# Optimization experiments

Hardware: AMD Instinct MI355X
Metric: run time of the kernel (lower is better)

The kernel has to match this reference:

```python
import jax, jax.numpy as jnp
import numpy as np

B = 131072
SD, AD, HID = 24, 8, 32
NH = SD + AD            # n_heads = 32
UNITS = HID * NH        # 1024


def _xavier(k, shape):
    fan_in, fan_out = shape[-2], shape[-1]
    lim = float(np.sqrt(6.0 / (fan_in + fan_out)))
    return jax.random.uniform(k, shape, jnp.float32, -lim, lim)


def setup_inputs() -> dict:
    key = jax.random.key(0)
    ks = jax.random.split(key, 8)
    return dict(
        state=jax.random.normal(ks[0], (B, SD), jnp.float32),
        action=jax.random.normal(ks[1], (B, AD), jnp.float32),
        # ripple layer 1: per-head Linear(NH -> HID), gate logits init 0 (init_prob=0.5)
        W1=_xavier(ks[2], (NH, NH, HID)), b1=jnp.zeros((NH, HID), jnp.float32), g1=jnp.zeros((NH,), jnp.float32),
        # ripple layer 2: per-head Linear(UNITS -> HID)
        W2=_xavier(ks[3], (NH, UNITS, HID)), b2=jnp.zeros((NH, HID), jnp.float32), g2=jnp.zeros((NH,), jnp.float32),
        # q_network
        Wq1=_xavier(ks[4], (UNITS, 256)), bq1=jnp.zeros((256,), jnp.float32),
        ln1_g=jnp.ones((256,), jnp.float32), ln1_b=jnp.zeros((256,), jnp.float32),
        Wq2=_xavier(ks[5], (256, 128)), bq2=jnp.zeros((128,), jnp.float32),
        ln2_g=jnp.ones((128,), jnp.float32), ln2_b=jnp.zeros((128,), jnp.float32),
        Wq3=_xavier(ks[6], (128, 1)), bq3=jnp.zeros((1,), jnp.float32),
    )


def _ripple(x, W, b, g):
    # x: [B, D]; W: [H, D, K]; per-head linear + tanh, scaled by per-head sigmoid gate
    h = jnp.tanh(jnp.einsum('bd,hdk->bhk', x, W) + b[None])  # [B, H, K]
    h = h * jax.nn.sigmoid(g)[None, :, None]
    return h.reshape(x.shape[0], -1)  # [B, H*K]


def _ln(x, g, b, eps=1e-5):
    mu = jnp.mean(x, -1, keepdims=True)
    var = jnp.mean((x - mu) ** 2, -1, keepdims=True)
    return (x - mu) * jax.lax.rsqrt(var + eps) * g + b


def reference(state, action, W1, b1, g1, W2, b2, g2,
              Wq1, bq1, ln1_g, ln1_b, Wq2, bq2, ln2_g, ln2_b, Wq3, bq3):
    sa = jnp.concatenate([state, action], axis=1)          # [B, SD+AD]
    x = _ripple(sa, W1, b1, g1)                            # [B, UNITS]
    x = _ripple(x, W2, b2, g2)                             # [B, UNITS]
    h = jax.nn.relu(_ln(x @ Wq1 + bq1, ln1_g, ln1_b))      # [B, 256] (dropout = eval identity)
    h = jax.nn.relu(_ln(h @ Wq2 + bq2, ln2_g, ln2_b))      # [B, 128]
    return h @ Wq3 + bq3                                   # [B, 1]
```

## Files before the change

### kernel.cpp

```cpp
#include <hip/hip_runtime.h>
#include <hip/hip_bf16.h>

typedef _Float16 f16x8 __attribute__((ext_vector_type(8)));
typedef float f32x4 __attribute__((ext_vector_type(4)));

__device__ __forceinline__ void async16(const _Float16* g, _Float16* l) {
  __builtin_amdgcn_global_load_lds(
      (const __attribute__((address_space(1))) unsigned int*)g,
      (__attribute__((address_space(3))) unsigned int*)l, 16, 0, 0);
}

__device__ __forceinline__ float tanh_fast(float x) {
  float e = __expf(2.0f * x);
  return 1.0f - 2.0f * __builtin_amdgcn_rcpf(e + 1.0f);
}
__device__ __forceinline__ float sigmoid_fast(float x) {
  return __builtin_amdgcn_rcpf(1.0f + __expf(-x));
}

__global__ __launch_bounds__(256) void transpose_cvt(const float* __restrict__ in,
                                                     _Float16* __restrict__ out,
                                                     int R, int C) {
  __shared__ float tile[32][33];
  int z = blockIdx.z;
  in  += (size_t)z * R * C;
  out += (size_t)z * R * C;
  int r0 = blockIdx.x * 32, c0 = blockIdx.y * 32;
  int t = threadIdx.x;
  int cc = t & 31, rr8 = t >> 5;
#pragma unroll
  for (int p = 0; p < 4; ++p) {
    int r = rr8 + p * 8;
    tile[cc][r] = in[(size_t)(r0 + r) * C + c0 + cc];
  }
  __syncthreads();
  int rr = t & 31, cc8 = t >> 5;
#pragma unroll
  for (int p = 0; p < 4; ++p) {
    int c = cc8 + p * 8;
    out[(size_t)(c0 + c) * R + r0 + rr] = (_Float16)tile[c][rr];
  }
}

__global__ __launch_bounds__(256) void k1_ripple1(
    const float* __restrict__ state, const float* __restrict__ action,
    const _Float16* __restrict__ v1t, const float* __restrict__ b1,
    const float* __restrict__ g1, _Float16* __restrict__ x1, int gro) {
  __shared__ __align__(16) _Float16 As[128 * 40];
  int bn = blockIdx.x, bm = blockIdx.y;
  int t = threadIdx.x, w = t >> 6, l = t & 63, q = l >> 4, l15 = l & 15;
  int n0 = bn * 128, m0 = bm * 128;

  {
    int r = t >> 1, half = t & 1;
    size_t grow = (size_t)(gro + m0 + r);
    float v[16];
    if (half == 0) {
      const float4* sp = (const float4*)(state + grow * 24);
      ((float4*)v)[0] = sp[0]; ((float4*)v)[1] = sp[1];
      ((float4*)v)[2] = sp[2]; ((float4*)v)[3] = sp[3];
    } else {
      const float4* sp = (const float4*)(state + grow * 24 + 16);
      ((float4*)v)[0] = sp[0]; ((float4*)v)[1] = sp[1];
      const float4* ap = (const float4*)(action + grow * 8);
      ((float4*)v)[2] = ap[0]; ((float4*)v)[3] = ap[1];
    }
    f16x8 h0, h1;
#pragma unroll
    for (int j = 0; j < 8; ++j) { h0[j] = (_Float16)v[j]; h1[j] = (_Float16)v[8 + j]; }
    *(f16x8*)&As[r * 40 + half * 16] = h0;
    *(f16x8*)&As[r * 40 + half * 16 + 8] = h1;
  }
  __syncthreads();

  int wr = w >> 1, wc = w & 1;
  f16x8 af[4], bf[4];
#pragma unroll
  for (int mi = 0; mi < 4; ++mi)
    af[mi] = *(const f16x8*)&As[(wr * 64 + mi * 16 + l15) * 40 + q * 8];
#pragma unroll
  for (int ni = 0; ni < 4; ++ni)
    bf[ni] = *(const f16x8*)(v1t + (size_t)(n0 + wc * 64 + ni * 16 + l15) * 32 + q * 8);

  f32x4 acc[4][4] = {};
#pragma unroll
  for (int mi = 0; mi < 4; ++mi)
#pragma unroll
    for (int ni = 0; ni < 4; ++ni)
      acc[mi][ni] = __builtin_amdgcn_mfma_f32_16x16x32_f16(af[mi], bf[ni], acc[mi][ni], 0, 0, 0);

#pragma unroll
  for (int ni = 0; ni < 4; ++ni) {
    int col = n0 + wc * 64 + ni * 16 + l15;
    float sg = sigmoid_fast(g1[col >> 5]);
    float bias = b1[col];
#pragma unroll
    for (int mi = 0; mi < 4; ++mi)
#pragma unroll
      for (int r = 0; r < 4; ++r) {
        int row = m0 + wr * 64 + mi * 16 + q * 4 + r;
        x1[(size_t)row * 1024 + col] = (_Float16)(tanh_fast(acc[mi][ni][r] + bias) * sg);
      }
  }
}

__global__ __launch_bounds__(256, 2) void k2_ripple2(
    const _Float16* __restrict__ x1, const _Float16* __restrict__ v2t,
    const float* __restrict__ b2, const float* __restrict__ g2,
    _Float16* __restrict__ x2, int nbm) {
  __shared__ __align__(16) _Float16 As[128 * 32];
  __shared__ __align__(16) _Float16 Bs[256 * 32];
  int g = blockIdx.x;
  int bn, bm;
  if ((nbm & 7) == 0) {
    int x = g & 7, j = g >> 3;
    bn = j & 3; bm = x + 8 * (j >> 2);
  } else { bn = g & 3; bm = g >> 2; }
  int t = threadIdx.x, w = t >> 6, l = t & 63, q = l >> 4, l15 = l & 15;
  int n0 = bn * 256, m0 = bm * 128;
  int wr = w >> 1, wc = w & 1;
  f32x4 acc[4][8] = {};

  int cA0 = t, cA1 = t + 256;
  const _Float16* aS0 = x1 + (size_t)(m0 + (cA0 >> 2)) * 1024 + ((cA0 & 3) ^ ((cA0 >> 3) & 3)) * 8;
  const _Float16* aS1 = x1 + (size_t)(m0 + (cA1 >> 2)) * 1024 + ((cA1 & 3) ^ ((cA1 >> 3) & 3)) * 8;
  _Float16* aD0 = As + cA0 * 8;
  _Float16* aD1 = As + cA1 * 8;
  const _Float16* bS[4]; _Float16* bD[4];
#pragma unroll
  for (int i = 0; i < 4; ++i) {
    int c = t + i * 256;
    bS[i] = v2t + (size_t)(n0 + (c >> 2)) * 1024 + ((c & 3) ^ ((c >> 3) & 3)) * 8;
    bD[i] = Bs + c * 8;
  }
  int qs = q ^ ((l15 >> 1) & 3);

  for (int kt = 0; kt < 32; ++kt) {
    __syncthreads();
    int ko = kt * 32;
    async16(aS0 + ko, aD0);
    async16(aS1 + ko, aD1);
#pragma unroll
    for (int i = 0; i < 4; ++i) async16(bS[i] + ko, bD[i]);
    __builtin_amdgcn_s_waitcnt(0);
    __syncthreads();
    f16x8 af[4], bf[8];
#pragma unroll
    for (int mi = 0; mi < 4; ++mi)
      af[mi] = *(const f16x8*)&As[(wr * 64 + mi * 16 + l15) * 32 + qs * 8];
#pragma unroll
    for (int ni = 0; ni < 8; ++ni)
      bf[ni] = *(const f16x8*)&Bs[(wc * 128 + ni * 16 + l15) * 32 + qs * 8];
#pragma unroll
    for (int mi = 0; mi < 4; ++mi)
#pragma unroll
      for (int ni = 0; ni < 8; ++ni)
        acc[mi][ni] = __builtin_amdgcn_mfma_f32_16x16x32_f16(af[mi], bf[ni], acc[mi][ni], 0, 0, 0);
  }

#pragma unroll
  for (int ni = 0; ni < 8; ++ni) {
    int col = n0 + wc * 128 + ni * 16 + l15;
    float sg = sigmoid_fast(g2[col >> 5]);
    float bias = b2[col];
#pragma unroll
    for (int mi = 0; mi < 4; ++mi)
#pragma unroll
      for (int r = 0; r < 4; ++r) {
        int row = m0 + wr * 64 + mi * 16 + q * 4 + r;
        x2[(size_t)row * 1024 + col] = (_Float16)(tanh_fast(acc[mi][ni][r] + bias) * sg);
      }
  }
}

__global__ __launch_bounds__(256) void k3_head(
    const _Float16* __restrict__ x2, const _Float16* __restrict__ t1t,
    const _Float16* __restrict__ t2t,
    const float* __restrict__ bq1, const float* __restrict__ ln1g, const float* __restrict__ ln1b,
    const float* __restrict__ bq2, const float* __restrict__ ln2g, const float* __restrict__ ln2b,
    const float* __restrict__ wq3, const float* __restrict__ bq3,
    float* __restrict__ out) {
  __shared__ __align__(16) _Float16 Ast[64 * 32];
  __shared__ __align__(16) _Float16 Bst[256 * 32];
  __shared__ __align__(16) _Float16 y1h[64 * 264];
  __shared__ float redA[64 * 4], redB[64 * 4];
  __shared__ float meanv[64], rstdv[64];
  int bm = blockIdx.x;
  int t = threadIdx.x, w = t >> 6, l = t & 63, q = l >> 4, l15 = l & 15;
  int m0 = bm * 64;
  int qs = q ^ ((l15 >> 1) & 3);

  f32x4 acc[4][4] = {};
  int cA = t;
  const _Float16* aS = x2 + (size_t)(m0 + (cA >> 2)) * 1024 + ((cA & 3) ^ ((cA >> 3) & 3)) * 8;
  _Float16* aD = Ast + cA * 8;
  const _Float16* bS[4]; _Float16* bD[4];
#pragma unroll
  for (int i = 0; i < 4; ++i) {
    int c = t + i * 256;
    bS[i] = t1t + (size_t)(c >> 2) * 1024 + ((c & 3) ^ ((c >> 3) & 3)) * 8;
    bD[i] = Bst + c * 8;
  }

  for (int kt = 0; kt < 32; ++kt) {
    __syncthreads();
    int ko = kt * 32;
    async16(aS + ko, aD);
#pragma unroll
    for (int i = 0; i < 4; ++i) async16(bS[i] + ko, bD[i]);
    __builtin_amdgcn_s_waitcnt(0);
    __syncthreads();
    f16x8 af[4], bf[4];
#pragma unroll
    for (int mi = 0; mi < 4; ++mi)
      af[mi] = *(const f16x8*)&Ast[(mi * 16 + l15) * 32 + qs * 8];
#pragma unroll
    for (int ni = 0; ni < 4; ++ni)
      bf[ni] = *(const f16x8*)&Bst[(w * 64 + ni * 16 + l15) * 32 + qs * 8];
#pragma unroll
    for (int mi = 0; mi < 4; ++mi)
#pragma unroll
      for (int ni = 0; ni < 4; ++ni)
        acc[mi][ni] = __builtin_amdgcn_mfma_f32_16x16x32_f16(af[mi], bf[ni], acc[mi][ni], 0, 0, 0);
  }

#pragma unroll
  for (int ni = 0; ni < 4; ++ni) {
    int col = w * 64 + ni * 16 + l15;
    float b = bq1[col];
#pragma unroll
    for (int mi = 0; mi < 4; ++mi)
#pragma unroll
      for (int r = 0; r < 4; ++r) acc[mi][ni][r] += b;
  }
#pragma unroll
  for (int mi = 0; mi < 4; ++mi)
#pragma unroll
    for (int r = 0; r < 4; ++r) {
      int row = mi * 16 + q * 4 + r;
      float s = 0.f, sq = 0.f;
#pragma unroll
      for (int ni = 0; ni < 4; ++ni) { float v = acc[mi][ni][r]; s += v; sq += v * v; }
#pragma unroll
      for (int off = 1; off < 16; off <<= 1) { s += __shfl_xor(s, off); sq += __shfl_xor(sq, off); }
      if (l15 == 0) { redA[row * 4 + w] = s; redB[row * 4 + w] = sq; }
    }
  __syncthreads();
  if (t < 64) {
    float s  = redA[t * 4] + redA[t * 4 + 1] + redA[t * 4 + 2] + redA[t * 4 + 3];
    float sq = redB[t * 4] + redB[t * 4 + 1] + redB[t * 4 + 2] + redB[t * 4 + 3];
    float mean = s * (1.0f / 256.0f);
    float var = sq * (1.0f / 256.0f) - mean * mean;
    meanv[t] = mean; rstdv[t] = rsqrtf(var + 1e-5f);
  }
  __syncthreads();
#pragma unroll
  for (int mi = 0; mi < 4; ++mi)
#pragma unroll
    for (int ni = 0; ni < 4; ++ni)
#pragma unroll
      for (int r = 0; r < 4; ++r) {
        int row = mi * 16 + q * 4 + r;
        int col = w * 64 + ni * 16 + l15;
        float y = (acc[mi][ni][r] - meanv[row]) * rstdv[row] * ln1g[col] + ln1b[col];
        y = fmaxf(y, 0.f);
        y1h[row * 264 + col] = (_Float16)y;
      }
  __syncthreads();

  int wr = w >> 1, wc = w & 1;
  f32x4 a2[2][4] = {};
  for (int kt = 0; kt < 8; ++kt) {
    f16x8 af2[2];
#pragma unroll
    for (int mi = 0; mi < 2; ++mi)
      af2[mi] = *(const f16x8*)&y1h[(wr * 32 + mi * 16 + l15) * 264 + kt * 32 + q * 8];
#pragma unroll
    for (int ni = 0; ni < 4; ++ni) {
      f16x8 bf = *(const f16x8*)(t2t + (size_t)(wc * 64 + ni * 16 + l15) * 256 + kt * 32 + q * 8);
#pragma unroll
      for (int mi = 0; mi < 2; ++mi)
        a2[mi][ni] = __builtin_amdgcn_mfma_f32_16x16x32_f16(af2[mi], bf, a2[mi][ni], 0, 0, 0);
    }
  }
#pragma unroll
  for (int ni = 0; ni < 4; ++ni) {
    int col = wc * 64 + ni * 16 + l15;
    float b = bq2[col];
#pragma unroll
    for (int mi = 0; mi < 2; ++mi)
#pragma unroll
      for (int r = 0; r < 4; ++r) a2[mi][ni][r] += b;
  }
  __syncthreads();
#pragma unroll
  for (int mi = 0; mi < 2; ++mi)
#pragma unroll
    for (int r = 0; r < 4; ++r) {
      int row = wr * 32 + mi * 16 + q * 4 + r;
      float s = 0.f, sq = 0.f;
#pragma unroll
      for (int ni = 0; ni < 4; ++ni) { float v = a2[mi][ni][r]; s += v; sq += v * v; }
#pragma unroll
      for (int off = 1; off < 16; off <<= 1) { s += __shfl_xor(s, off); sq += __shfl_xor(sq, off); }
      if (l15 == 0) { redA[row * 2 + wc] = s; redB[row * 2 + wc] = sq; }
    }
  __syncthreads();
  if (t < 64) {
    float s = redA[t * 2] + redA[t * 2 + 1];
    float sq = redB[t * 2] + redB[t * 2 + 1];
    float mean = s * (1.0f / 128.0f);
    float var = sq * (1.0f / 128.0f) - mean * mean;
    meanv[t] = mean; rstdv[t] = rsqrtf(var + 1e-5f);
  }
  __syncthreads();
#pragma unroll
  for (int mi = 0; mi < 2; ++mi)
#pragma unroll
    for (int r = 0; r < 4; ++r) {
      int row = wr * 32 + mi * 16 + q * 4 + r;
      float pr = 0.f;
#pragma unroll
      for (int ni = 0; ni < 4; ++ni) {
        int col = wc * 64 + ni * 16 + l15;
        float y = (a2[mi][ni][r] - meanv[row]) * rstdv[row] * ln2g[col] + ln2b[col];
        y = fmaxf(y, 0.f);
        pr += y * wq3[col];
      }
#pragma unroll
      for (int off = 1; off < 16; off <<= 1) pr += __shfl_xor(pr, off);
      if (l15 == 0) redA[row * 2 + wc] = pr;
    }
  __syncthreads();
  if (t < 64) out[m0 + t] = redA[t * 2] + redA[t * 2 + 1] + bq3[0];
}

extern "C" void kernel_launch(void* const* d_in, const int* in_sizes, int n_in,
                              void* d_out, int out_size, void* d_ws, size_t ws_size,
                              hipStream_t stream) {
  const float* state  = (const float*)d_in[0];
  const float* action = (const float*)d_in[1];
  const float* W1  = (const float*)d_in[2];
  const float* b1  = (const float*)d_in[3];
  const float* g1  = (const float*)d_in[4];
  const float* W2  = (const float*)d_in[5];
  const float* b2  = (const float*)d_in[6];
  const float* g2  = (const float*)d_in[7];
  const float* Wq1 = (const float*)d_in[8];
  const float* bq1 = (const float*)d_in[9];
  const float* ln1g = (const float*)d_in[10];
  const float* ln1b = (const float*)d_in[11];
  const float* Wq2 = (const float*)d_in[12];
  const float* bq2 = (const float*)d_in[13];
  const float* ln2g = (const float*)d_in[14];
  const float* ln2b = (const float*)d_in[15];
  const float* Wq3 = (const float*)d_in[16];
  const float* bq3 = (const float*)d_in[17];
  int B = in_sizes[0] / 24;

  char* ws = (char*)d_ws;
  _Float16* V1t = (_Float16*)(ws);
  _Float16* V2t = (_Float16*)(ws + 65536);
  _Float16* T1t = (_Float16*)(ws + 65536 + 2097152);
  _Float16* T2t = (_Float16*)(ws + 65536 + 2097152 + 524288);
  size_t woff = (65536 + 2097152 + 524288 + 65536 + 4095) & ~(size_t)4095;

  size_t avail = ws_size > woff ? ws_size - woff : 0;
  long rows = (long)(avail / 4096);
  if (rows > 32768) rows = 32768;
  rows &= ~127L;
  if (rows < 128) rows = 128;
  int S = (int)rows;
  _Float16* x1 = (_Float16*)(ws + woff);
  _Float16* x2 = x1 + (size_t)S * 1024;

  transpose_cvt<<<dim3(1, 1, 32), 256, 0, stream>>>(W1, V1t, 32, 32);
  transpose_cvt<<<dim3(32, 1, 32), 256, 0, stream>>>(W2, V2t, 1024, 32);
  transpose_cvt<<<dim3(32, 8, 1), 256, 0, stream>>>(Wq1, T1t, 1024, 256);
  transpose_cvt<<<dim3(8, 4, 1), 256, 0, stream>>>(Wq2, T2t, 256, 128);

  for (int r0 = 0; r0 < B; r0 += S) {
    int Sc = S < (B - r0) ? S : (B - r0);
    int nbm = Sc / 128;
    k1_ripple1<<<dim3(8, nbm), 256, 0, stream>>>(state, action, V1t, b1, g1, x1, r0);
    k2_ripple2<<<dim3(4 * nbm), 256, 0, stream>>>(x1, V2t, b2, g2, x2, nbm);
    k3_head<<<dim3(Sc / 64), 256, 0, stream>>>(x2, T1t, T2t, bq1, ln1g, ln1b,
                                               bq2, ln2g, ln2b, Wq3, bq3,
                                               (float*)d_out + r0);
  }
}
```

Before: 697.5 us.

## Shrink ripple2 tile to 128x128 and double K-step per barrier in head GEMM

The ripple-2 GEMM tile shrinks from 128x256 to 128x128. This halves accumulator registers and shared memory so three blocks can fit per CU, and it doubles the grid with an updated block swizzle. The head kernel now loads two 32-wide K slices per iteration into doubled shared buffers, which halves the number of barrier/wait rounds. The costs are more redundant A-tile loads in ripple2, since each A tile is now fetched by eight column blocks instead of four, and larger shared memory use in the head kernel.

```diff
diff --git a/kernel.cpp b/kernel.cpp
--- a/kernel.cpp
+++ b/kernel.cpp
@@ -104,35 +104,30 @@
   }
 }
 
-__global__ __launch_bounds__(256, 2) void k2_ripple2(
+__global__ __launch_bounds__(256, 3) void k2_ripple2(
     const _Float16* __restrict__ x1, const _Float16* __restrict__ v2t,
     const float* __restrict__ b2, const float* __restrict__ g2,
     _Float16* __restrict__ x2, int nbm) {
   __shared__ __align__(16) _Float16 As[128 * 32];
-  __shared__ __align__(16) _Float16 Bs[256 * 32];
+  __shared__ __align__(16) _Float16 Bs[128 * 32];
   int g = blockIdx.x;
   int bn, bm;
   if ((nbm & 7) == 0) {
     int x = g & 7, j = g >> 3;
-    bn = j & 3; bm = x + 8 * (j >> 2);
-  } else { bn = g & 3; bm = g >> 2; }
+    bn = j & 7; bm = x + 8 * (j >> 3);
+  } else { bn = g & 7; bm = g >> 3; }
   int t = threadIdx.x, w = t >> 6, l = t & 63, q = l >> 4, l15 = l & 15;
-  int n0 = bn * 256, m0 = bm * 128;
+  int n0 = bn * 128, m0 = bm * 128;
   int wr = w >> 1, wc = w & 1;
-  f32x4 acc[4][8] = {};
-
-  int cA0 = t, cA1 = t + 256;
-  const _Float16* aS0 = x1 + (size_t)(m0 + (cA0 >> 2)) * 1024 + ((cA0 & 3) ^ ((cA0 >> 3) & 3)) * 8;
-  const _Float16* aS1 = x1 + (size_t)(m0 + (cA1 >> 2)) * 1024 + ((cA1 & 3) ^ ((cA1 >> 3) & 3)) * 8;
-  _Float16* aD0 = As + cA0 * 8;
-  _Float16* aD1 = As + cA1 * 8;
-  const _Float16* bS[4]; _Float16* bD[4];
-#pragma unroll
-  for (int i = 0; i < 4; ++i) {
-    int c = t + i * 256;
-    bS[i] = v2t + (size_t)(n0 + (c >> 2)) * 1024 + ((c & 3) ^ ((c >> 3) & 3)) * 8;
-    bD[i] = Bs + c * 8;
-  }
+  f32x4 acc[4][4] = {};
+
+  int c0 = t, c1 = t + 256;
+  const _Float16* aS0 = x1 + (size_t)(m0 + (c0 >> 2)) * 1024 + ((c0 & 3) ^ ((c0 >> 3) & 3)) * 8;
+  const _Float16* aS1 = x1 + (size_t)(m0 + (c1 >> 2)) * 1024 + ((c1 & 3) ^ ((c1 >> 3) & 3)) * 8;
+  const _Float16* bS0 = v2t + (size_t)(n0 + (c0 >> 2)) * 1024 + ((c0 & 3) ^ ((c0 >> 3) & 3)) * 8;
+  const _Float16* bS1 = v2t + (size_t)(n0 + (c1 >> 2)) * 1024 + ((c1 & 3) ^ ((c1 >> 3) & 3)) * 8;
+  _Float16* aD0 = As + c0 * 8; _Float16* aD1 = As + c1 * 8;
+  _Float16* bD0 = Bs + c0 * 8; _Float16* bD1 = Bs + c1 * 8;
   int qs = q ^ ((l15 >> 1) & 3);
 
   for (int kt = 0; kt < 32; ++kt) {
@@ -140,27 +135,27 @@
     int ko = kt * 32;
     async16(aS0 + ko, aD0);
     async16(aS1 + ko, aD1);
-#pragma unroll
-    for (int i = 0; i < 4; ++i) async16(bS[i] + ko, bD[i]);
+    async16(bS0 + ko, bD0);
+    async16(bS1 + ko, bD1);
     __builtin_amdgcn_s_waitcnt(0);
     __syncthreads();
-    f16x8 af[4], bf[8];
+    f16x8 af[4], bf[4];
 #pragma unroll
     for (int mi = 0; mi < 4; ++mi)
       af[mi] = *(const f16x8*)&As[(wr * 64 + mi * 16 + l15) * 32 + qs * 8];
 #pragma unroll
-    for (int ni = 0; ni < 8; ++ni)
-      bf[ni] = *(const f16x8*)&Bs[(wc * 128 + ni * 16 + l15) * 32 + qs * 8];
-#pragma unroll
-    for (int mi = 0; mi < 4; ++mi)
-#pragma unroll
-      for (int ni = 0; ni < 8; ++ni)
+    for (int ni = 0; ni < 4; ++ni)
+      bf[ni] = *(const f16x8*)&Bs[(wc * 64 + ni * 16 + l15) * 32 + qs * 8];
+#pragma unroll
+    for (int mi = 0; mi < 4; ++mi)
+#pragma unroll
+      for (int ni = 0; ni < 4; ++ni)
         acc[mi][ni] = __builtin_amdgcn_mfma_f32_16x16x32_f16(af[mi], bf[ni], acc[mi][ni], 0, 0, 0);
   }
 
 #pragma unroll
-  for (int ni = 0; ni < 8; ++ni) {
-    int col = n0 + wc * 128 + ni * 16 + l15;
+  for (int ni = 0; ni < 4; ++ni) {
+    int col = n0 + wc * 64 + ni * 16 + l15;
     float sg = sigmoid_fast(g2[col >> 5]);
     float bias = b2[col];
 #pragma unroll
@@ -180,8 +175,8 @@
     const float* __restrict__ bq2, const float* __restrict__ ln2g, const float* __restrict__ ln2b,
     const float* __restrict__ wq3, const float* __restrict__ bq3,
     float* __restrict__ out) {
-  __shared__ __align__(16) _Float16 Ast[64 * 32];
-  __shared__ __align__(16) _Float16 Bst[256 * 32];
+  __shared__ __align__(16) _Float16 Ast[2 * 64 * 32];
+  __shared__ __align__(16) _Float16 Bst[2 * 256 * 32];
   __shared__ __align__(16) _Float16 y1h[64 * 264];
   __shared__ float redA[64 * 4], redB[64 * 4];
   __shared__ float meanv[64], rstdv[64];
@@ -202,26 +197,33 @@
     bD[i] = Bst + c * 8;
   }
 
-  for (int kt = 0; kt < 32; ++kt) {
+  for (int kt = 0; kt < 16; ++kt) {
     __syncthreads();
-    int ko = kt * 32;
+    int ko = kt * 64;
     async16(aS + ko, aD);
-#pragma unroll
-    for (int i = 0; i < 4; ++i) async16(bS[i] + ko, bD[i]);
+    async16(aS + ko + 32, aD + 64 * 32);
+#pragma unroll
+    for (int i = 0; i < 4; ++i) {
+      async16(bS[i] + ko, bD[i]);
+      async16(bS[i] + ko + 32, bD[i] + 256 * 32);
+    }
     __builtin_amdgcn_s_waitcnt(0);
     __syncthreads();
-    f16x8 af[4], bf[4];
-#pragma unroll
-    for (int mi = 0; mi < 4; ++mi)
-      af[mi] = *(const f16x8*)&Ast[(mi * 16 + l15) * 32 + qs * 8];
-#pragma unroll
-    for (int ni = 0; ni < 4; ++ni)
-      bf[ni] = *(const f16x8*)&Bst[(w * 64 + ni * 16 + l15) * 32 + qs * 8];
-#pragma unroll
-    for (int mi = 0; mi < 4; ++mi)
+#pragma unroll
+    for (int s = 0; s < 2; ++s) {
+      f16x8 af[4], bf[4];
+#pragma unroll
+      for (int mi = 0; mi < 4; ++mi)
+        af[mi] = *(const f16x8*)&Ast[s * 2048 + (mi * 16 + l15) * 32 + qs * 8];
 #pragma unroll
       for (int ni = 0; ni < 4; ++ni)
-        acc[mi][ni] = __builtin_amdgcn_mfma_f32_16x16x32_f16(af[mi], bf[ni], acc[mi][ni], 0, 0, 0);
+        bf[ni] = *(const f16x8*)&Bst[s * 8192 + (w * 64 + ni * 16 + l15) * 32 + qs * 8];
+#pragma unroll
+      for (int mi = 0; mi < 4; ++mi)
+#pragma unroll
+        for (int ni = 0; ni < 4; ++ni)
+          acc[mi][ni] = __builtin_amdgcn_mfma_f32_16x16x32_f16(af[mi], bf[ni], acc[mi][ni], 0, 0, 0);
+    }
   }
 
 #pragma unroll
@@ -383,7 +385,7 @@
     int Sc = S < (B - r0) ? S : (B - r0);
     int nbm = Sc / 128;
     k1_ripple1<<<dim3(8, nbm), 256, 0, stream>>>(state, action, V1t, b1, g1, x1, r0);
-    k2_ripple2<<<dim3(4 * nbm), 256, 0, stream>>>(x1, V2t, b2, g2, x2, nbm);
+    k2_ripple2<<<dim3(8 * nbm), 256, 0, stream>>>(x1, V2t, b2, g2, x2, nbm);
     k3_head<<<dim3(Sc / 64), 256, 0, stream>>>(x2, T1t, T2t, bq1, ln1g, ln1b,
                                                bq2, ln2g, ln2b, Wq3, bq3,
                                                (float*)d_out + r0);
```

Measured after the change: 702.6 us. Within noise of the previous version (+0.7%).
